# Kernel optimization log

Hardware: AMD Instinct MI355X
Metric: run time of the kernel (lower is better)

## Reference

```python
import jax, jax.numpy as jnp
import numpy as np

# norse LIFParameters defaults with v_th overridden to 0.23
DT = 1e-3
TAU_SYN_INV = 200.0   # 1/5e-3
TAU_MEM_INV = 100.0   # 1/1e-2
V_TH = 0.23
ENC_V_TH = 1.0        # encoder uses default LIFParameters (v_th=1.0)
SEQ_LEN = 24
HIDDEN = 256
N_CLASSES = 10


def heaviside(x):
    return (x > 0).astype(x.dtype)


def encode(x):
    """ConstantCurrentLIFEncoder: lif_current_encoder over SEQ_LEN steps. x: [B, F] -> [T, B, F] spikes."""
    def step(v, _):
        v = v + DT * TAU_MEM_INV * (x - v)          # dv = dt*tau_mem_inv*((v_leak - v) + I)
        z = heaviside(v - ENC_V_TH)
        v = (1.0 - z) * v                            # reset to v_reset = 0
        return v, z
    _, zs = jax.lax.scan(step, jnp.zeros_like(x), None, length=SEQ_LEN)
    return zs


def lif_ff_step(inp, v, i):
    """norse lif_feed_forward_step: decay v with old i, decay i, spike, reset, then add input to i."""
    v_dec = v + DT * TAU_MEM_INV * (i - v)           # v_leak = 0
    i_dec = i * (1.0 - DT * TAU_SYN_INV)
    z = heaviside(v_dec - V_TH)
    v_new = (1.0 - z) * v_dec                        # v_reset = 0
    i_new = i_dec + inp
    return z, v_new, i_new


def setup_inputs() -> dict:
    key = jax.random.key(0)
    ks = jax.random.split(key, 8)
    B, F = 4096, 1024
    def lin(k, fan_in, fan_out):
        bound = 1.0 / np.sqrt(fan_in)
        kw, kb = jax.random.split(k)
        W = jax.random.uniform(kw, (fan_out, fan_in), jnp.float32, -bound, bound)
        b = jax.random.uniform(kb, (fan_out,), jnp.float32, -bound, bound)
        return W, b
    x = jax.random.normal(ks[0], (B, F), jnp.float32)
    W1, b1 = lin(ks[1], F, HIDDEN)
    W2, b2 = lin(ks[2], HIDDEN, HIDDEN)
    W3, b3 = lin(ks[3], HIDDEN, HIDDEN)
    Wli = jax.random.normal(ks[4], (N_CLASSES, HIDDEN), jnp.float32) * np.sqrt(2.0 / HIDDEN)
    return {"x": x, "W1": W1, "b1": b1, "W2": W2, "b2": b2, "W3": W3, "b3": b3, "Wli": Wli}


def reference(x, W1, b1, W2, b2, W3, b3, Wli):
    # dropout layers are identity in eval mode
    enc = encode(x)                                   # [T, B, F]
    B = x.shape[0]
    z2 = lambda d: jnp.zeros((B, d), x.dtype)
    carry0 = (z2(HIDDEN), z2(HIDDEN), z2(HIDDEN), z2(HIDDEN), z2(HIDDEN), z2(HIDDEN),
              z2(N_CLASSES), z2(N_CLASSES))
    def step(c, z):
        v1, i1, v2, i2, v3, i3, vo, io = c
        o1, v1, i1 = lif_ff_step(z @ W1.T + b1, v1, i1)
        o2, v2, i2 = lif_ff_step(o1 @ W2.T + b2, v2, i2)
        o2 = o2 + o1                                  # residual
        o3, v3, i3 = lif_ff_step(o2 @ W3.T + b3, v3, i3)
        o3 = o3 + o2                                  # residual
        # LILinearCell li_step: v from old i, i decays then accumulates W @ input (no bias)
        vo = vo + DT * TAU_MEM_INV * (io - vo)
        io = io * (1.0 - DT * TAU_SYN_INV) + o3 @ Wli.T
        return (v1, i1, v2, i2, v3, i3, vo, io), vo
    _, voltages = jax.lax.scan(step, carry0, enc)     # [T, B, n_classes]
    return voltages[-1]                               # decode = last timestep
```

## Files before the change

kernel.cpp:

```cpp
#include <hip/hip_runtime.h>
#include <hip/hip_bf16.h>

#define FEAT   1024
#define HID    256
#define TSTEPS 24
#define NCLS   10

typedef unsigned int u32;
typedef unsigned long long u64;
typedef unsigned short u16;
typedef float v2f __attribute__((ext_vector_type(2)));

constexpr int OFF_W1T  = 0;
constexpr int OFF_W2T  = OFF_W1T + FEAT*HID;
constexpr int OFF_W3T  = OFF_W2T + HID*HID;
constexpr int OFF_WLI  = OFF_W3T + HID*HID;
constexpr int OFF_B1   = OFF_WLI + NCLS*HID;
constexpr int OFF_B2   = OFF_B1 + HID;
constexpr int OFF_B3   = OFF_B2 + HID;

struct CoefT { float c[TSTEPS]; };
constexpr CoefT make_coef() {
    CoefT r{};
    double c = 0.0, p9 = 1.0;
    r.c[TSTEPS-1] = 0.0f;
    for (int u = TSTEPS-1; u > 0; u--) {
        c = 0.8 * c + 0.1 * p9;
        p9 *= 0.9;
        r.c[u-1] = (float)c;
    }
    return r;
}
__device__ constexpr CoefT COEF = make_coef();

__device__ __forceinline__ u32 detect_bf16(const void* __restrict__ x, u32 lane) {
    float v = __bfloat162float(((const __hip_bfloat16*)x)[lane]);
    u64 bad = __ballot(!(fabsf(v) < 100.0f));
    return bad == 0ull ? 1u : 0u;
}

__device__ __forceinline__ float rd_any(const void* p, int idx, u32 isbf) {
    return isbf ? __bfloat162float(((const __hip_bfloat16*)p)[idx])
                : ((const float*)p)[idx];
}

__device__ __forceinline__ float4 rd4(const void* p, int i, u32 isbf) {
    if (isbf) {
        const u32* q = (const u32*)p;
        u32 a = q[i >> 1], b = q[(i >> 1) + 1];
        float4 r;
        r.x = __uint_as_float(a << 16); r.y = __uint_as_float(a & 0xffff0000u);
        r.z = __uint_as_float(b << 16); r.w = __uint_as_float(b & 0xffff0000u);
        return r;
    }
    return ((const float4*)p)[i >> 2];
}

__global__ __launch_bounds__(256) void prep_k(const void* __restrict__ x,
        const void* W1, const void* W2, const void* W3, const void* Wli,
        const void* b1, const void* b2, const void* b3, float* __restrict__ ws) {
    const u32 isbf = detect_bf16(x, threadIdx.x & 63);
    int b = blockIdx.x;
    const u32 t = threadIdx.x;
    if (b < 256) {
        int id = b * 256 + t;
        int h = id >> 8, f4 = (id & 255) << 2;
        float4 w = rd4(W1, h * FEAT + f4, isbf);
        float* d = ws + OFF_W1T;
        d[(f4+0)*HID + h] = w.x; d[(f4+1)*HID + h] = w.y;
        d[(f4+2)*HID + h] = w.z; d[(f4+3)*HID + h] = w.w;
        return;
    }
    b -= 256;
    if (b < 64) {
        int id = b * 256 + t;
        int h = id >> 6, f4 = (id & 63) << 2;
        float4 w = rd4(W2, h * HID + f4, isbf);
        float* d = ws + OFF_W2T;
        d[(f4+0)*HID + h] = w.x; d[(f4+1)*HID + h] = w.y;
        d[(f4+2)*HID + h] = w.z; d[(f4+3)*HID + h] = w.w;
        return;
    }
    b -= 64;
    if (b < 64) {
        int id = b * 256 + t;
        int h = id >> 6, f4 = (id & 63) << 2;
        float4 w = rd4(W3, h * HID + f4, isbf);
        float* d = ws + OFF_W3T;
        d[(f4+0)*HID + h] = w.x; d[(f4+1)*HID + h] = w.y;
        d[(f4+2)*HID + h] = w.z; d[(f4+3)*HID + h] = w.w;
        return;
    }
    for (u32 e = t; e < NCLS*HID; e += 256) ws[OFF_WLI + e] = rd_any(Wli, e, isbf);
    ws[OFF_B1 + t] = rd_any(b1, t, isbf);
    ws[OFF_B2 + t] = rd_any(b2, t, isbf);
    ws[OFF_B3 + t] = rd_any(b3, t, isbf);
}

__device__ __forceinline__ u32 mbcnt64(u64 m) {
    return __builtin_amdgcn_mbcnt_hi((u32)(m >> 32),
           __builtin_amdgcn_mbcnt_lo((u32)m, 0u));
}


__device__ __forceinline__ u32 build_list4(u16* list, u32 lmA, u32 lmB, u32 lane) {
    u32 u = lmA | lmB;
    u32 cnt = (u32)__builtin_popcount(u);
    u64 B0 = __ballot((cnt & 1u) != 0);
    u64 B1 = __ballot((cnt & 2u) != 0);
    u64 B2 = __ballot((cnt & 4u) != 0);
    u32 pos = mbcnt64(B0) + 2u*mbcnt64(B1) + 4u*mbcnt64(B2);
    u32 n = (u32)__builtin_popcountll(B0) + 2u*(u32)__builtin_popcountll(B1)
          + 4u*(u32)__builtin_popcountll(B2);
    while (u) {
        u32 j = (u32)__builtin_ctz(u); u &= u - 1;
        u32 mult = ((lmA >> j) & 1u) + ((lmB >> j) & 1u);
        list[pos++] = (u16)(((lane << 2) + j) | (mult << 12));
    }
    u32 pad = (8u - (n & 7u)) & 7u;
    if (lane < pad) list[n + lane] = 0;
    return n;
}

__device__ __forceinline__ u32 build_listE(u16* list, u32 lm, u32 lane) {
    u32 cnt = (u32)__builtin_popcount(lm);
    u32 pos = 0, n = 0;
    #pragma unroll
    for (int b = 0; b < 5; b++) {
        u64 B = __ballot(((cnt >> b) & 1u) != 0);
        pos += mbcnt64(B) << b;
        n += ((u32)__builtin_popcountll(B)) << b;
    }
    while (lm) {
        u32 j = (u32)__builtin_ctz(lm); lm &= lm - 1;
        list[pos++] = (u16)(((lane << 4) + j) | 0x1000u);
    }
    u32 pad = (8u - (n & 7u)) & 7u;
    if (lane < pad) list[n + lane] = 0;
    return n;
}

#define GSTEP(E, W) do { \
    float mm = (float)((E) >> 12); \
    v2f mv = {mm, mm}; \
    v2f lo = {(W).x, (W).y}, hi = {(W).z, (W).w}; \
    accA += mv * lo; accB += mv * hi; \
} while (0)

__device__ __forceinline__ void gather_list(v2f& accA, v2f& accB,
        const float* __restrict__ Wt, const u16* list, u32 n, u32 lane4) {
    u32 nch = (n + 7u) >> 3;
    const uint4* lp = (const uint4*)list;
    for (u32 c = 0; c < nch; c++) {
        uint4 d = lp[c];
        u32 e0 = d.x & 0xffffu, e1 = d.x >> 16;
        u32 e2 = d.y & 0xffffu, e3 = d.y >> 16;
        u32 e4 = d.z & 0xffffu, e5 = d.z >> 16;
        u32 e6 = d.w & 0xffffu, e7 = d.w >> 16;
        const float4 w0 = *(const float4*)(Wt + ((e0 & 0xfffu) << 8) + lane4);
        const float4 w1 = *(const float4*)(Wt + ((e1 & 0xfffu) << 8) + lane4);
        const float4 w2 = *(const float4*)(Wt + ((e2 & 0xfffu) << 8) + lane4);
        const float4 w3 = *(const float4*)(Wt + ((e3 & 0xfffu) << 8) + lane4);
        const float4 w4 = *(const float4*)(Wt + ((e4 & 0xfffu) << 8) + lane4);
        const float4 w5 = *(const float4*)(Wt + ((e5 & 0xfffu) << 8) + lane4);
        const float4 w6 = *(const float4*)(Wt + ((e6 & 0xfffu) << 8) + lane4);
        const float4 w7 = *(const float4*)(Wt + ((e7 & 0xfffu) << 8) + lane4);
        GSTEP(e0, w0); GSTEP(e1, w1); GSTEP(e2, w2); GSTEP(e3, w3);
        GSTEP(e4, w4); GSTEP(e5, w5); GSTEP(e6, w6); GSTEP(e7, w7);
    }
}

__global__ __launch_bounds__(256) void snn_k(const void* __restrict__ xin,
                                             const float* __restrict__ ws,
                                             void* __restrict__ out) {
    const u32 tid  = threadIdx.x;
    const u32 lane = tid & 63;
    const u32 wv   = tid >> 6;
    const int row  = blockIdx.x * 4 + wv;
    const u32 lane4 = lane * 4;
    const u32 isbf = detect_bf16(xin, lane);

    const float* __restrict__ W1T = ws + OFF_W1T;
    const float* __restrict__ W2T = ws + OFF_W2T;
    const float* __restrict__ W3T = ws + OFF_W3T;
    const float* __restrict__ WLI = ws + OFF_WLI;

    __shared__ u32 sched[12 * 256];
    __shared__ __align__(16) u16 listE[4][1040];
    __shared__ __align__(16) u16 listL[4][272];

    {
        float xv[16];
        if (isbf) {
            const uint4* xp = (const uint4*)((const u16*)xin + (size_t)row*FEAT + lane*16);
            uint4 A = xp[0], B = xp[1];
            u32 w[8] = {A.x, A.y, A.z, A.w, B.x, B.y, B.z, B.w};
            #pragma unroll
            for (int i = 0; i < 8; i++) {
                xv[2*i]   = __uint_as_float(w[i] << 16);
                xv[2*i+1] = __uint_as_float(w[i] & 0xffff0000u);
            }
        } else {
            const float4* xp = (const float4*)((const float*)xin + (size_t)row*FEAT + lane*16);
            float4 A = xp[0], B = xp[1], C = xp[2], D = xp[3];
            float tmp[16] = {A.x,A.y,A.z,A.w,B.x,B.y,B.z,B.w,C.x,C.y,C.z,C.w,D.x,D.y,D.z,D.w};
            #pragma unroll
            for (int i = 0; i < 16; i++) xv[i] = tmp[i];
        }
        u32 smreg[12];
        #pragma unroll
        for (int i = 0; i < 12; i++) smreg[i] = 0;
        #pragma unroll
        for (int j = 0; j < 16; j++) {
            float v = 0.f;
            #pragma unroll
            for (int t = 0; t < TSTEPS; t++) {
                v = v + 0.1f * (xv[j] - v);
                bool z = v > 1.0f;
                v = z ? 0.0f : v;
                if (z) smreg[t >> 1] |= 1u << (((t & 1) << 4) + j);
            }
        }
        #pragma unroll
        for (int i = 0; i < 12; i++) sched[i * 256 + tid] = smreg[i];
    }

    float v1[4], i1[4], v2[4], i2[4], v3[4], i3[4], g[4];
    #pragma unroll
    for (int k = 0; k < 4; k++) {
        v1[k]=0.f; i1[k]=0.f; v2[k]=0.f; i2[k]=0.f; v3[k]=0.f; i3[k]=0.f; g[k]=0.f;
    }
    const float4 b1v = *(const float4*)(ws + OFF_B1 + lane4);
    const float4 b2v = *(const float4*)(ws + OFF_B2 + lane4);
    const float4 b3v = *(const float4*)(ws + OFF_B3 + lane4);

    u16* const lE = listE[wv];
    u16* const lL = listL[wv];

    u32 pairreg = 0;
    for (int t = 0; t < TSTEPS; t++) {
        if ((t & 1) == 0) pairreg = sched[(t >> 1) * 256 + tid];
        const u32 lmE = (t & 1) ? (pairreg >> 16) : (pairreg & 0xffffu);

        u32 nE = build_listE(lE, lmE, lane);
        v2f accA = {b1v.x, b1v.y}, accB = {b1v.z, b1v.w};
        gather_list(accA, accB, W1T, lE, nE, lane4);
        float a1[4] = {accA.x, accA.y, accB.x, accB.y};

        float o1v[4]; u32 lm1 = 0;
        #pragma unroll
        for (int kk = 0; kk < 4; kk++) {
            float vd = v1[kk] + 0.1f * (i1[kk] - v1[kk]);
            i1[kk] = i1[kk] * 0.8f;
            bool z = vd > 0.23f;
            v1[kk] = z ? 0.0f : vd;
            i1[kk] = i1[kk] + a1[kk];
            o1v[kk] = z ? 1.0f : 0.0f;
            lm1 |= (z ? 1u : 0u) << kk;
        }

        u32 n1 = build_list4(lL, lm1, 0u, lane);
        accA = (v2f){b2v.x, b2v.y}; accB = (v2f){b2v.z, b2v.w};
        gather_list(accA, accB, W2T, lL, n1, lane4);
        float a2[4] = {accA.x, accA.y, accB.x, accB.y};

        float o2v[4]; u32 lm2 = 0;
        #pragma unroll
        for (int kk = 0; kk < 4; kk++) {
            float vd = v2[kk] + 0.1f * (i2[kk] - v2[kk]);
            i2[kk] = i2[kk] * 0.8f;
            bool z = vd > 0.23f;
            v2[kk] = z ? 0.0f : vd;
            i2[kk] = i2[kk] + a2[kk];
            o2v[kk] = (z ? 1.0f : 0.0f) + o1v[kk];
            lm2 |= (z ? 1u : 0u) << kk;
        }

        u32 n2 = build_list4(lL, lm1, lm2, lane);
        accA = (v2f){b3v.x, b3v.y}; accB = (v2f){b3v.z, b3v.w};
        gather_list(accA, accB, W3T, lL, n2, lane4);
        float a3[4] = {accA.x, accA.y, accB.x, accB.y};

        const float cf = COEF.c[t];
        #pragma unroll
        for (int kk = 0; kk < 4; kk++) {
            float vd = v3[kk] + 0.1f * (i3[kk] - v3[kk]);
            i3[kk] = i3[kk] * 0.8f;
            bool z = vd > 0.23f;
            v3[kk] = z ? 0.0f : vd;
            i3[kk] = i3[kk] + a3[kk];
            float o3 = (z ? 1.0f : 0.0f) + o2v[kk];
            g[kk] += cf * o3;
        }
    }

    float s[NCLS];
    #pragma unroll
    for (int c = 0; c < NCLS; c++) {
        const float4 w = *(const float4*)(WLI + c*HID + lane4);
        float p = g[0]*w.x + g[1]*w.y + g[2]*w.z + g[3]*w.w;
        #pragma unroll
        for (int d = 32; d > 0; d >>= 1) p += __shfl_xor(p, d, 64);
        s[c] = p;
    }
    if (lane == 0) {
        if (isbf) {
            __hip_bfloat16* o = (__hip_bfloat16*)out + (size_t)row*NCLS;
            #pragma unroll
            for (int c = 0; c < NCLS; c++) o[c] = __float2bfloat16(s[c]);
        } else {
            float* o = (float*)out + (size_t)row*NCLS;
            #pragma unroll
            for (int c = 0; c < NCLS; c++) o[c] = s[c];
        }
    }
}

extern "C" void kernel_launch(void* const* d_in, const int* in_sizes, int n_in,
                              void* d_out, int out_size, void* d_ws, size_t ws_size,
                              hipStream_t stream) {
    const void* x   = d_in[0];
    const void* W1  = d_in[1];
    const void* b1  = d_in[2];
    const void* W2  = d_in[3];
    const void* b2  = d_in[4];
    const void* W3  = d_in[5];
    const void* b3  = d_in[6];
    const void* Wli = d_in[7];
    float* ws = (float*)d_ws;
    const int batch = in_sizes[0] / FEAT;

    prep_k<<<385, 256, 0, stream>>>(x, W1, W2, W3, Wli, b1, b2, b3, ws);
    snn_k<<<batch/4, 256, 0, stream>>>(x, ws, d_out);
}
```

Baseline: 156.8 us.

## Use byte-offset spike lists with zero-row padding and tiled weight transpose

```diff
diff --git a/kernel.cpp b/kernel.cpp
--- a/kernel.cpp
+++ b/kernel.cpp
@@ -12,12 +12,15 @@
 typedef float v2f __attribute__((ext_vector_type(2)));
 
 constexpr int OFF_W1T  = 0;
-constexpr int OFF_W2T  = OFF_W1T + FEAT*HID;
-constexpr int OFF_W3T  = OFF_W2T + HID*HID;
-constexpr int OFF_WLI  = OFF_W3T + HID*HID;
+constexpr int OFF_W2T  = OFF_W1T + 1025*HID;
+constexpr int OFF_W3T  = OFF_W2T + 257*HID;
+constexpr int OFF_WLI  = OFF_W3T + 257*HID;
 constexpr int OFF_B1   = OFF_WLI + NCLS*HID;
 constexpr int OFF_B2   = OFF_B1 + HID;
 constexpr int OFF_B3   = OFF_B2 + HID;
+
+constexpr u32 ZPAD1 = 1024u << 10;
+constexpr u32 ZPAD2 = 256u  << 10;
 
 struct CoefT { float c[TSTEPS]; };
 constexpr CoefT make_coef() {
@@ -60,69 +63,51 @@
         const void* W1, const void* W2, const void* W3, const void* Wli,
         const void* b1, const void* b2, const void* b3, float* __restrict__ ws) {
     const u32 isbf = detect_bf16(x, threadIdx.x & 63);
+    const u32 t = threadIdx.x;
     int b = blockIdx.x;
-    const u32 t = threadIdx.x;
-    if (b < 256) {
-        int id = b * 256 + t;
-        int h = id >> 8, f4 = (id & 255) << 2;
-        float4 w = rd4(W1, h * FEAT + f4, isbf);
-        float* d = ws + OFF_W1T;
-        d[(f4+0)*HID + h] = w.x; d[(f4+1)*HID + h] = w.y;
-        d[(f4+2)*HID + h] = w.z; d[(f4+3)*HID + h] = w.w;
+
+    if (b == 384) {
+        for (u32 e = t; e < NCLS*HID; e += 256) ws[OFF_WLI + e] = rd_any(Wli, e, isbf);
+        ws[OFF_B1 + t] = rd_any(b1, t, isbf);
+        ws[OFF_B2 + t] = rd_any(b2, t, isbf);
+        ws[OFF_B3 + t] = rd_any(b3, t, isbf);
+        ws[OFF_W1T + 1024*HID + t] = 0.f;
+        ws[OFF_W2T + 256*HID + t] = 0.f;
+        ws[OFF_W3T + 256*HID + t] = 0.f;
         return;
     }
-    b -= 256;
-    if (b < 64) {
-        int id = b * 256 + t;
-        int h = id >> 6, f4 = (id & 63) << 2;
-        float4 w = rd4(W2, h * HID + f4, isbf);
-        float* d = ws + OFF_W2T;
-        d[(f4+0)*HID + h] = w.x; d[(f4+1)*HID + h] = w.y;
-        d[(f4+2)*HID + h] = w.z; d[(f4+3)*HID + h] = w.w;
-        return;
-    }
-    b -= 64;
-    if (b < 64) {
-        int id = b * 256 + t;
-        int h = id >> 6, f4 = (id & 63) << 2;
-        float4 w = rd4(W3, h * HID + f4, isbf);
-        float* d = ws + OFF_W3T;
-        d[(f4+0)*HID + h] = w.x; d[(f4+1)*HID + h] = w.y;
-        d[(f4+2)*HID + h] = w.z; d[(f4+3)*HID + h] = w.w;
-        return;
-    }
-    for (u32 e = t; e < NCLS*HID; e += 256) ws[OFF_WLI + e] = rd_any(Wli, e, isbf);
-    ws[OFF_B1 + t] = rd_any(b1, t, isbf);
-    ws[OFF_B2 + t] = rd_any(b2, t, isbf);
-    ws[OFF_B3 + t] = rd_any(b3, t, isbf);
+
+    const void* src; float* dst; int srcW, h0, f0;
+    if (b < 256)      { src = W1; dst = ws + OFF_W1T; srcW = FEAT; h0 = (b >> 5) * 32; f0 = (b & 31) * 32; }
+    else if (b < 320) { int tb = b - 256; src = W2; dst = ws + OFF_W2T; srcW = HID; h0 = (tb >> 3) * 32; f0 = (tb & 7) * 32; }
+    else              { int tb = b - 320; src = W3; dst = ws + OFF_W3T; srcW = HID; h0 = (tb >> 3) * 32; f0 = (tb & 7) * 32; }
+
+    __shared__ float sm[32 * 36];
+    {
+        u32 r = t >> 3, c4 = (t & 7) * 4;
+        float4 w = rd4(src, (h0 + r) * srcW + f0 + c4, isbf);
+        *(float4*)&sm[r * 36 + c4] = w;
+    }
+    __syncthreads();
+    {
+        u32 f = t >> 3, h4 = (t & 7) * 4;
+        float4 o;
+        o.x = sm[(h4 + 0) * 36 + f];
+        o.y = sm[(h4 + 1) * 36 + f];
+        o.z = sm[(h4 + 2) * 36 + f];
+        o.w = sm[(h4 + 3) * 36 + f];
+        *(float4*)&dst[(size_t)(f0 + f) * HID + h0 + h4] = o;
+    }
 }
 
 __device__ __forceinline__ u32 mbcnt64(u64 m) {
     return __builtin_amdgcn_mbcnt_hi((u32)(m >> 32),
            __builtin_amdgcn_mbcnt_lo((u32)m, 0u));
 }
-
-
-__device__ __forceinline__ u32 build_list4(u16* list, u32 lmA, u32 lmB, u32 lane) {
-    u32 u = lmA | lmB;
-    u32 cnt = (u32)__builtin_popcount(u);
-    u64 B0 = __ballot((cnt & 1u) != 0);
-    u64 B1 = __ballot((cnt & 2u) != 0);
-    u64 B2 = __ballot((cnt & 4u) != 0);
-    u32 pos = mbcnt64(B0) + 2u*mbcnt64(B1) + 4u*mbcnt64(B2);
-    u32 n = (u32)__builtin_popcountll(B0) + 2u*(u32)__builtin_popcountll(B1)
-          + 4u*(u32)__builtin_popcountll(B2);
-    while (u) {
-        u32 j = (u32)__builtin_ctz(u); u &= u - 1;
-        u32 mult = ((lmA >> j) & 1u) + ((lmB >> j) & 1u);
-        list[pos++] = (u16)(((lane << 2) + j) | (mult << 12));
-    }
-    u32 pad = (8u - (n & 7u)) & 7u;
-    if (lane < pad) list[n + lane] = 0;
-    return n;
-}
-
-__device__ __forceinline__ u32 build_listE(u16* list, u32 lm, u32 lane) {
+__device__ __forceinline__ u32 round8(u32 n) { return (n + 7u) & ~7u; }
+
+
+__device__ __forceinline__ u32 build_listE(u32* list, u32 lm, u32 lane) {
     u32 cnt = (u32)__builtin_popcount(lm);
     u32 pos = 0, n = 0;
     #pragma unroll
@@ -133,40 +118,55 @@
     }
     while (lm) {
         u32 j = (u32)__builtin_ctz(lm); lm &= lm - 1;
-        list[pos++] = (u16)(((lane << 4) + j) | 0x1000u);
-    }
-    u32 pad = (8u - (n & 7u)) & 7u;
-    if (lane < pad) list[n + lane] = 0;
-    return n;
-}
-
-#define GSTEP(E, W) do { \
-    float mm = (float)((E) >> 12); \
-    v2f mv = {mm, mm}; \
-    v2f lo = {(W).x, (W).y}, hi = {(W).z, (W).w}; \
-    accA += mv * lo; accB += mv * hi; \
-} while (0)
-
-__device__ __forceinline__ void gather_list(v2f& accA, v2f& accB,
-        const float* __restrict__ Wt, const u16* list, u32 n, u32 lane4) {
-    u32 nch = (n + 7u) >> 3;
+        list[pos++] = ((lane << 4) + j) << 10;
+    }
+    u32 np = round8(n);
+    if (lane < np - n) list[n + lane] = ZPAD1;
+    return np;
+}
+
+__device__ __forceinline__ u32 build_listZ(u32* list, u32 lm, u32 start, u32 lane) {
+    u32 cnt = (u32)__builtin_popcount(lm);
+    u64 B0 = __ballot((cnt & 1u) != 0);
+    u64 B1 = __ballot((cnt & 2u) != 0);
+    u64 B2 = __ballot((cnt & 4u) != 0);
+    u32 pos = start + mbcnt64(B0) + 2u*mbcnt64(B1) + 4u*mbcnt64(B2);
+    u32 n = start + (u32)__builtin_popcountll(B0) + 2u*(u32)__builtin_popcountll(B1)
+          + 4u*(u32)__builtin_popcountll(B2);
+    while (lm) {
+        u32 j = (u32)__builtin_ctz(lm); lm &= lm - 1;
+        list[pos++] = ((lane << 2) + j) << 10;
+    }
+    u32 np = round8(n);
+    if (lane < np - n) list[n + lane] = ZPAD2;
+    return np;
+}
+
+__device__ __forceinline__ void gather(v2f& A, v2f& B, const float* __restrict__ Wt,
+                                       const u32* __restrict__ list, u32 np, u32 lane16) {
+    const char* __restrict__ base = (const char*)Wt;
     const uint4* lp = (const uint4*)list;
+    u32 nch = np >> 3;
     for (u32 c = 0; c < nch; c++) {
-        uint4 d = lp[c];
-        u32 e0 = d.x & 0xffffu, e1 = d.x >> 16;
-        u32 e2 = d.y & 0xffffu, e3 = d.y >> 16;
-        u32 e4 = d.z & 0xffffu, e5 = d.z >> 16;
-        u32 e6 = d.w & 0xffffu, e7 = d.w >> 16;
-        const float4 w0 = *(const float4*)(Wt + ((e0 & 0xfffu) << 8) + lane4);
-        const float4 w1 = *(const float4*)(Wt + ((e1 & 0xfffu) << 8) + lane4);
-        const float4 w2 = *(const float4*)(Wt + ((e2 & 0xfffu) << 8) + lane4);
-        const float4 w3 = *(const float4*)(Wt + ((e3 & 0xfffu) << 8) + lane4);
-        const float4 w4 = *(const float4*)(Wt + ((e4 & 0xfffu) << 8) + lane4);
-        const float4 w5 = *(const float4*)(Wt + ((e5 & 0xfffu) << 8) + lane4);
-        const float4 w6 = *(const float4*)(Wt + ((e6 & 0xfffu) << 8) + lane4);
-        const float4 w7 = *(const float4*)(Wt + ((e7 & 0xfffu) << 8) + lane4);
-        GSTEP(e0, w0); GSTEP(e1, w1); GSTEP(e2, w2); GSTEP(e3, w3);
-        GSTEP(e4, w4); GSTEP(e5, w5); GSTEP(e6, w6); GSTEP(e7, w7);
+        uint4 d0 = lp[2*c], d1 = lp[2*c + 1];
+        u32 a0 = d0.x + lane16, a1 = d0.y + lane16, a2 = d0.z + lane16, a3 = d0.w + lane16;
+        u32 a4 = d1.x + lane16, a5 = d1.y + lane16, a6 = d1.z + lane16, a7 = d1.w + lane16;
+        const float4 w0 = *(const float4*)(base + a0);
+        const float4 w1 = *(const float4*)(base + a1);
+        const float4 w2 = *(const float4*)(base + a2);
+        const float4 w3 = *(const float4*)(base + a3);
+        const float4 w4 = *(const float4*)(base + a4);
+        const float4 w5 = *(const float4*)(base + a5);
+        const float4 w6 = *(const float4*)(base + a6);
+        const float4 w7 = *(const float4*)(base + a7);
+        A += (v2f){w0.x, w0.y}; B += (v2f){w0.z, w0.w};
+        A += (v2f){w1.x, w1.y}; B += (v2f){w1.z, w1.w};
+        A += (v2f){w2.x, w2.y}; B += (v2f){w2.z, w2.w};
+        A += (v2f){w3.x, w3.y}; B += (v2f){w3.z, w3.w};
+        A += (v2f){w4.x, w4.y}; B += (v2f){w4.z, w4.w};
+        A += (v2f){w5.x, w5.y}; B += (v2f){w5.z, w5.w};
+        A += (v2f){w6.x, w6.y}; B += (v2f){w6.z, w6.w};
+        A += (v2f){w7.x, w7.y}; B += (v2f){w7.z, w7.w};
     }
 }
 
@@ -177,7 +177,7 @@
     const u32 lane = tid & 63;
     const u32 wv   = tid >> 6;
     const int row  = blockIdx.x * 4 + wv;
-    const u32 lane4 = lane * 4;
+    const u32 lane16 = lane * 16;
     const u32 isbf = detect_bf16(xin, lane);
 
     const float* __restrict__ W1T = ws + OFF_W1T;
@@ -186,8 +186,8 @@
     const float* __restrict__ WLI = ws + OFF_WLI;
 
     __shared__ u32 sched[12 * 256];
-    __shared__ __align__(16) u16 listE[4][1040];
-    __shared__ __align__(16) u16 listL[4][272];
+    __shared__ __align__(16) u32 listE[4][1032];
+    __shared__ __align__(16) u32 listL[4][528];
 
     {
         float xv[16];
@@ -230,12 +230,13 @@
     for (int k = 0; k < 4; k++) {
         v1[k]=0.f; i1[k]=0.f; v2[k]=0.f; i2[k]=0.f; v3[k]=0.f; i3[k]=0.f; g[k]=0.f;
     }
+    const u32 lane4 = lane * 4;
     const float4 b1v = *(const float4*)(ws + OFF_B1 + lane4);
     const float4 b2v = *(const float4*)(ws + OFF_B2 + lane4);
     const float4 b3v = *(const float4*)(ws + OFF_B3 + lane4);
 
-    u16* const lE = listE[wv];
-    u16* const lL = listL[wv];
+    u32* const lE = listE[wv];
+    u32* const lL = listL[wv];
 
     u32 pairreg = 0;
     for (int t = 0; t < TSTEPS; t++) {
@@ -244,7 +245,7 @@
 
         u32 nE = build_listE(lE, lmE, lane);
         v2f accA = {b1v.x, b1v.y}, accB = {b1v.z, b1v.w};
-        gather_list(accA, accB, W1T, lE, nE, lane4);
+        gather(accA, accB, W1T, lE, nE, lane16);
         float a1[4] = {accA.x, accA.y, accB.x, accB.y};
 
         float o1v[4]; u32 lm1 = 0;
@@ -259,9 +260,9 @@
             lm1 |= (z ? 1u : 0u) << kk;
         }
 
-        u32 n1 = build_list4(lL, lm1, 0u, lane);
+        u32 n1p = build_listZ(lL, lm1, 0u, lane);
         accA = (v2f){b2v.x, b2v.y}; accB = (v2f){b2v.z, b2v.w};
-        gather_list(accA, accB, W2T, lL, n1, lane4);
+        gather(accA, accB, W2T, lL, n1p, lane16);
         float a2[4] = {accA.x, accA.y, accB.x, accB.y};
 
         float o2v[4]; u32 lm2 = 0;
@@ -276,9 +277,9 @@
             lm2 |= (z ? 1u : 0u) << kk;
         }
 
-        u32 n2 = build_list4(lL, lm1, lm2, lane);
+        u32 nend = build_listZ(lL, lm2, n1p, lane);
         accA = (v2f){b3v.x, b3v.y}; accB = (v2f){b3v.z, b3v.w};
-        gather_list(accA, accB, W3T, lL, n2, lane4);
+        gather(accA, accB, W3T, lL, nend, lane16);
         float a3[4] = {accA.x, accA.y, accB.x, accB.y};
 
         const float cf = COEF.c[t];
```

New measurement: 165.4 us. +5.5%, slower.
